# Optimization experiments

Measured on AMD Instinct MI355X. Metric: run time of the kernel, lower is better.

Reference implementation:

```python
import jax, jax.numpy as jnp
import numpy as np

N_NODES = 50000
N_EDGES = 800000
IN_FEATS = 128
H_FEATS = 128
OUT_FEATS = 64


def _mean_agg(h, src, dst, n_nodes):
    # mean over in-neighbors: sum h[src] into dst, divide by in-degree (0 for isolated nodes)
    summed = jax.ops.segment_sum(h[src], dst, num_segments=n_nodes)  # [N, d]
    deg = jax.ops.segment_sum(jnp.ones((src.shape[0],), h.dtype), dst, num_segments=n_nodes)
    return summed / jnp.maximum(deg, 1.0)[:, None]


def setup_inputs() -> dict:
    key = jax.random.key(0)
    ks = jax.random.split(key, 10)
    s = 0.05
    return {
        "inputs": jax.random.normal(ks[0], (N_NODES, IN_FEATS), jnp.float32),
        "fc_W": jax.random.normal(ks[1], (H_FEATS, IN_FEATS), jnp.float32) * s,
        "fc_b": jax.random.normal(ks[2], (H_FEATS,), jnp.float32) * s,
        "W": jax.random.normal(ks[3], (3, H_FEATS, H_FEATS), jnp.float32) * s,
        "b": jax.random.normal(ks[4], (3, H_FEATS), jnp.float32) * s,
        "W_last": jax.random.normal(ks[5], (OUT_FEATS, H_FEATS), jnp.float32) * s,
        "b_last": jax.random.normal(ks[6], (OUT_FEATS,), jnp.float32) * s,
        "eps": jnp.zeros((4,), jnp.float32),
        "src": jax.random.randint(ks[7], (N_EDGES,), 0, N_NODES, jnp.int32),
        "dst": jax.random.randint(ks[8], (N_EDGES,), 0, N_NODES, jnp.int32),
    }


def reference(inputs, fc_W, fc_b, W, b, W_last, b_last, eps, src, dst):
    n = inputs.shape[0]
    # input SLP
    h = jax.nn.relu(inputs @ fc_W.T + fc_b)
    # 3 hidden GIN layers: relu(Linear((1+eps)*h + mean_agg(h)))  (dropout = eval identity)
    for i in range(3):
        agg = _mean_agg(h, src, dst, n)
        h = jax.nn.relu(((1.0 + eps[i]) * h + agg) @ W[i].T + b[i])
    # last GIN layer (no ReLU)
    agg = _mean_agg(h, src, dst, n)
    h = ((1.0 + eps[3]) * h + agg) @ W_last.T + b_last
    return h
```

## Files before the change

### kernel.cpp

```cpp
#include <hip/hip_runtime.h>

#define N_NODES 50000
#define N_EDGES 800000
#define NBUCK 196
#define CAP 4608
#define EPB 4096
#define NSTRIPE ((N_EDGES + EPB - 1) / EPB)

typedef __attribute__((ext_vector_type(8))) short short8;
typedef __attribute__((ext_vector_type(4))) float float4v;

__device__ inline unsigned short f2bf(float f) {
    unsigned u = __float_as_uint(f);
    unsigned r = u + 0x7fff + ((u >> 16) & 1);
    return (unsigned short)(r >> 16);
}
__device__ inline float bf2f(unsigned short h) {
    return __uint_as_float(((unsigned)h) << 16);
}


__global__ void __launch_bounds__(256) wsplit_init(
    const float* __restrict__ fcW, const float* __restrict__ W, const float* __restrict__ Wl,
    unsigned short* __restrict__ hi, unsigned short* __restrict__ lo, int* __restrict__ cursor) {
    if (blockIdx.x == 0 && threadIdx.x < NBUCK) cursor[threadIdx.x] = threadIdx.x * CAP;
    int i = blockIdx.x * 256 + threadIdx.x;
    float v;
    if (i < 16384) v = fcW[i];
    else if (i < 65536) v = W[i - 16384];
    else if (i < 73728) v = Wl[i - 65536];
    else return;
    unsigned short h = f2bf(v);
    hi[i] = h;
    lo[i] = f2bf(v - bf2f(h));
}


__global__ void bucket_scan(const int* __restrict__ cursor, int* __restrict__ boff,
                            int* __restrict__ row_ptr) {
    __shared__ int sm[256];
    int t = threadIdx.x;
    int v = (t < NBUCK) ? (cursor[t] - t * CAP) : 0;
    sm[t] = v;
    __syncthreads();
    for (int o = 1; o < 256; o <<= 1) {
        int x = sm[t];
        int a = (t >= o) ? sm[t - o] : 0;
        __syncthreads();
        sm[t] = x + a;
        __syncthreads();
    }
    if (t < NBUCK) boff[t] = sm[t] - v;
    if (t == NBUCK - 1) {
        boff[NBUCK] = sm[t];
        row_ptr[N_NODES] = sm[t];
    }
}


template <int COLS, bool RELU, bool WRITE_BF, bool BIAS, bool ASPLIT>
__device__ __forceinline__ void gemm_body(int bx, const float* __restrict__ U,
                                          const unsigned short* __restrict__ Uhi,
                                          const unsigned short* __restrict__ Ulo,
                                          const unsigned short* __restrict__ Whi,
                                          const unsigned short* __restrict__ Wlo,
                                          const float* __restrict__ bias, float* __restrict__ out,
                                          unsigned short* __restrict__ outbf, int nrows) {
    int wave = threadIdx.x >> 6;
    int lane = threadIdx.x & 63;
    int m = lane & 15;
    int quad = lane >> 4;
    int r0 = bx * 64 + wave * 16;
    int rowA = r0 + m;
    if (rowA >= nrows) rowA = nrows - 1;

    short8 ahi[4], alo[4];
    if (ASPLIT) {
        const unsigned short* hp = Uhi + (size_t)rowA * 128 + quad * 8;
        const unsigned short* lp = Ulo + (size_t)rowA * 128 + quad * 8;
#pragma unroll
        for (int kc = 0; kc < 4; kc++) {
            ahi[kc] = *(const short8*)(hp + kc * 32);
            alo[kc] = *(const short8*)(lp + kc * 32);
        }
    } else {
        const float* arow = U + (size_t)rowA * 128 + quad * 8;
#pragma unroll
        for (int kc = 0; kc < 4; kc++) {
            float4 f0 = *(const float4*)(arow + kc * 32);
            float4 f1 = *(const float4*)(arow + kc * 32 + 4);
            float fv[8] = {f0.x, f0.y, f0.z, f0.w, f1.x, f1.y, f1.z, f1.w};
#pragma unroll
            for (int j = 0; j < 8; j++) {
                unsigned short h = f2bf(fv[j]);
                ahi[kc][j] = (short)h;
                alo[kc][j] = (short)f2bf(fv[j] - bf2f(h));
            }
        }
    }

#pragma unroll
    for (int nt = 0; nt < COLS / 16; nt++) {
        int n = nt * 16 + m;
        const unsigned short* bhp = Whi + (size_t)n * 128 + quad * 8;
        const unsigned short* blp = Wlo + (size_t)n * 128 + quad * 8;
        float4v acc = {0.f, 0.f, 0.f, 0.f};
#pragma unroll
        for (int kc = 0; kc < 4; kc++) {
            short8 bh = *(const short8*)(bhp + kc * 32);
            short8 bl = *(const short8*)(blp + kc * 32);
            acc = __builtin_amdgcn_mfma_f32_16x16x32_bf16(ahi[kc], bh, acc, 0, 0, 0);
            acc = __builtin_amdgcn_mfma_f32_16x16x32_bf16(alo[kc], bh, acc, 0, 0, 0);
            acc = __builtin_amdgcn_mfma_f32_16x16x32_bf16(ahi[kc], bl, acc, 0, 0, 0);
        }
        float bv = 0.f;
        if (BIAS) bv = bias[n];
#pragma unroll
        for (int i = 0; i < 4; i++) {
            int r = r0 + quad * 4 + i;
            if (r < nrows) {
                float v = acc[i] + bv;
                if (RELU) v = fmaxf(v, 0.f);
                out[(size_t)r * COLS + n] = v;
                if (WRITE_BF) outbf[(size_t)r * COLS + n] = f2bf(v);
            }
        }
    }
}

template <int COLS, bool RELU, bool WRITE_BF, bool BIAS, bool ASPLIT>
__global__ void __launch_bounds__(256) gemm_mfma(const float* __restrict__ U,
                                                 const unsigned short* __restrict__ Uhi,
                                                 const unsigned short* __restrict__ Ulo,
                                                 const unsigned short* __restrict__ Whi,
                                                 const unsigned short* __restrict__ Wlo,
                                                 const float* __restrict__ bias,
                                                 float* __restrict__ out,
                                                 unsigned short* __restrict__ outbf, int nrows) {
    gemm_body<COLS, RELU, WRITE_BF, BIAS, ASPLIT>(blockIdx.x, U, Uhi, Ulo, Whi, Wlo, bias, out,
                                                  outbf, nrows);
}


__global__ void __launch_bounds__(256) fused_binA_gemm(
    const int* __restrict__ src, const int* __restrict__ dst, int* __restrict__ cursor,
    int* __restrict__ packed, const float* __restrict__ X, const unsigned short* __restrict__ whi,
    const unsigned short* __restrict__ wlo, const float* __restrict__ fcb, float* __restrict__ h,
    unsigned short* __restrict__ hbf) {
    int bx = blockIdx.x;
    if (bx < NSTRIPE) {
        __shared__ int lcount[256];
        __shared__ int lbase[256];
        int t = threadIdx.x;
        lcount[t] = 0;
        __syncthreads();
        int base = bx * EPB + t;
#pragma unroll 4
        for (int k = 0; k < EPB / 256; k++) {
            int i = base + k * 256;
            if (i < N_EDGES) atomicAdd(&lcount[((unsigned)dst[i]) >> 8], 1);
        }
        __syncthreads();
        if (t < NBUCK) {
            lbase[t] = atomicAdd(&cursor[t], lcount[t]);
            lcount[t] = 0;
        }
        __syncthreads();
#pragma unroll 4
        for (int k = 0; k < EPB / 256; k++) {
            int i = base + k * 256;
            if (i < N_EDGES) {
                int d = dst[i];
                int wb = ((unsigned)d) >> 8;
                int p = lbase[wb] + atomicAdd(&lcount[wb], 1);
                if (p < (wb + 1) * CAP)
                    packed[p] = ((d & 255) << 16) | src[i];
            }
        }
    } else {
        gemm_body<128, true, true, true, false>(bx - NSTRIPE, X, nullptr, nullptr, whi, wlo, fcb,
                                                h, hbf, N_NODES);
    }
}


__global__ void __launch_bounds__(256) binB_kernel(const int* __restrict__ packed,
                                                   const int* __restrict__ cursor,
                                                   const int* __restrict__ boff,
                                                   int* __restrict__ row_ptr,
                                                   int* __restrict__ esrc) {
    __shared__ int sm[256];
    __shared__ int curs[256];
    int b = blockIdx.x;
    int t = threadIdx.x;
    int e0r = b * CAP, e1r = cursor[b];
    int w0 = boff[b];
    curs[t] = 0;
    __syncthreads();
    for (int i = e0r + t; i < e1r; i += 256) atomicAdd(&curs[((unsigned)packed[i]) >> 16], 1);
    __syncthreads();
    int v = curs[t];
    sm[t] = v;
    __syncthreads();
    for (int o = 1; o < 256; o <<= 1) {
        int x = sm[t];
        int a = (t >= o) ? sm[t - o] : 0;
        __syncthreads();
        sm[t] = x + a;
        __syncthreads();
    }
    int excl = sm[t] - v;
    curs[t] = excl;
    int node = b * 256 + t;
    if (node < N_NODES) row_ptr[node] = w0 + excl;
    __syncthreads();
    for (int i = e0r + t; i < e1r; i += 256) {
        unsigned w = (unsigned)packed[i];
        int p = atomicAdd(&curs[w >> 16], 1);
        esrc[w0 + p] = (int)(w & 0xFFFFu);
    }
}


__global__ void __launch_bounds__(256) agg_kernel(
    const float* __restrict__ h, const unsigned short* __restrict__ hbf,
    const int* __restrict__ row_ptr, const int* __restrict__ esrc,
    const float* __restrict__ eps, int layer, unsigned* __restrict__ uhi32,
    unsigned* __restrict__ ulo32) {
    int gtid = blockIdx.x * 256 + threadIdx.x;
    int node = gtid >> 6;
    int lane = threadIdx.x & 63;
    if (node >= N_NODES) return;
    node = __builtin_amdgcn_readfirstlane(node);
    int beg = __builtin_amdgcn_readfirstlane(row_ptr[node]);
    int end = __builtin_amdgcn_readfirstlane(row_ptr[node + 1]);
    int eg = lane >> 4;
    int fo = lane & 15;

    float acc[8] = {0.f, 0.f, 0.f, 0.f, 0.f, 0.f, 0.f, 0.f};
    int e = beg;
#pragma unroll 2
    for (; e + 3 < end; e += 4) {
        int s = esrc[e + eg];
        short8 v = *(const short8*)(hbf + (size_t)s * 128 + fo * 8);
#pragma unroll
        for (int j = 0; j < 8; j++) acc[j] += bf2f((unsigned short)v[j]);
    }
    int rem = end - e;
    if (eg < rem) {
        int s = esrc[e + eg];
        short8 v = *(const short8*)(hbf + (size_t)s * 128 + fo * 8);
#pragma unroll
        for (int j = 0; j < 8; j++) acc[j] += bf2f((unsigned short)v[j]);
    }
#pragma unroll
    for (int j = 0; j < 8; j++) {
        acc[j] += __shfl_xor(acc[j], 16);
        acc[j] += __shfl_xor(acc[j], 32);
    }
    if (eg == 0) {
        int d = end - beg;
        float inv = (d > 0) ? 1.0f / (float)d : 0.0f;
        float ep = 1.0f + eps[layer];
        const float* hr = h + (size_t)node * 128 + fo * 8;
        float4 h0 = *(const float4*)hr;
        float4 h1 = *(const float4*)(hr + 4);
        float hv[8] = {h0.x, h0.y, h0.z, h0.w, h1.x, h1.y, h1.z, h1.w};
        unsigned hip[4], lop[4];
#pragma unroll
        for (int jj = 0; jj < 4; jj++) {
            float ux = ep * hv[2 * jj] + acc[2 * jj] * inv;
            float uy = ep * hv[2 * jj + 1] + acc[2 * jj + 1] * inv;
            unsigned short uh0 = f2bf(ux), uh1 = f2bf(uy);
            hip[jj] = (unsigned)uh0 | ((unsigned)uh1 << 16);
            lop[jj] = (unsigned)f2bf(ux - bf2f(uh0)) | ((unsigned)f2bf(uy - bf2f(uh1)) << 16);
        }
        uint4* ph = (uint4*)(uhi32 + (size_t)node * 64 + fo * 4);
        uint4* pl = (uint4*)(ulo32 + (size_t)node * 64 + fo * 4);
        *ph = make_uint4(hip[0], hip[1], hip[2], hip[3]);
        *pl = make_uint4(lop[0], lop[1], lop[2], lop[3]);
    }
}


__global__ void __launch_bounds__(256) agg64_out(
    const float* __restrict__ g, const unsigned short* __restrict__ gbf,
    const int* __restrict__ row_ptr, const int* __restrict__ esrc,
    const float* __restrict__ eps, const float* __restrict__ bl, float* __restrict__ out) {
    int gtid = blockIdx.x * 256 + threadIdx.x;
    int node = gtid >> 6;
    if (node >= N_NODES) return;
    int lane = threadIdx.x & 63;
    node = __builtin_amdgcn_readfirstlane(node);
    int beg = __builtin_amdgcn_readfirstlane(row_ptr[node]);
    int end = __builtin_amdgcn_readfirstlane(row_ptr[node + 1]);
    int eg = lane >> 3;
    int fo = lane & 7;

    float acc[8] = {0.f, 0.f, 0.f, 0.f, 0.f, 0.f, 0.f, 0.f};
    int e = beg;
#pragma unroll 2
    for (; e + 7 < end; e += 8) {
        int s = esrc[e + eg];
        short8 v = *(const short8*)(gbf + (size_t)s * 64 + fo * 8);
#pragma unroll
        for (int j = 0; j < 8; j++) acc[j] += bf2f((unsigned short)v[j]);
    }
    int rem = end - e;
    if (eg < rem) {
        int s = esrc[e + eg];
        short8 v = *(const short8*)(gbf + (size_t)s * 64 + fo * 8);
#pragma unroll
        for (int j = 0; j < 8; j++) acc[j] += bf2f((unsigned short)v[j]);
    }
#pragma unroll
    for (int j = 0; j < 8; j++) {
        acc[j] += __shfl_xor(acc[j], 8);
        acc[j] += __shfl_xor(acc[j], 16);
        acc[j] += __shfl_xor(acc[j], 32);
    }
    if (eg == 0) {
        int d = end - beg;
        float inv = (d > 0) ? 1.0f / (float)d : 0.0f;
        float ep = 1.0f + eps[3];
        const float* gr = g + (size_t)node * 64 + fo * 8;
        float4 g0 = *(const float4*)gr;
        float4 g1 = *(const float4*)(gr + 4);
        const float* blr = bl + fo * 8;
        float4 b0 = *(const float4*)blr;
        float4 b1 = *(const float4*)(blr + 4);
        float4 r0, r1;
        r0.x = ep * g0.x + acc[0] * inv + b0.x;
        r0.y = ep * g0.y + acc[1] * inv + b0.y;
        r0.z = ep * g0.z + acc[2] * inv + b0.z;
        r0.w = ep * g0.w + acc[3] * inv + b0.w;
        r1.x = ep * g1.x + acc[4] * inv + b1.x;
        r1.y = ep * g1.y + acc[5] * inv + b1.y;
        r1.z = ep * g1.z + acc[6] * inv + b1.z;
        r1.w = ep * g1.w + acc[7] * inv + b1.w;
        float* op = out + (size_t)node * 64 + fo * 8;
        *(float4*)op = r0;
        *(float4*)(op + 4) = r1;
    }
}


extern "C" void kernel_launch(void* const* d_in, const int* in_sizes, int n_in,
                              void* d_out, int out_size, void* d_ws, size_t ws_size,
                              hipStream_t stream) {
    const float* X   = (const float*)d_in[0];
    const float* fcW = (const float*)d_in[1];
    const float* fcb = (const float*)d_in[2];
    const float* W   = (const float*)d_in[3];
    const float* b   = (const float*)d_in[4];
    const float* Wl  = (const float*)d_in[5];
    const float* bl  = (const float*)d_in[6];
    const float* eps = (const float*)d_in[7];
    const int* src   = (const int*)d_in[8];
    const int* dst   = (const int*)d_in[9];
    float* out = (float*)d_out;

    float* h = (float*)d_ws;
    unsigned short* hbf = (unsigned short*)(h + (size_t)N_NODES * 128);
    unsigned short* uhi = hbf + (size_t)N_NODES * 128;
    unsigned short* ulo = uhi + (size_t)N_NODES * 128;
    unsigned short* whi = ulo + (size_t)N_NODES * 128;
    unsigned short* wlo = whi + 73728;
    int* cursor  = (int*)(wlo + 73728);
    int* boff    = cursor + NBUCK;
    int* row_ptr = boff + NBUCK + 1;
    int* packed  = row_ptr + N_NODES + 1;
    int* esrc    = packed + NBUCK * CAP;
    float* g = (float*)uhi;
    unsigned short* gbf = ulo;

    const int gemm_blocks = (N_NODES + 63) / 64;
    const int agg_blocks = (N_NODES * 64 + 255) / 256;
    const int prep_blocks = (73728 + 255) / 256;

    wsplit_init<<<prep_blocks, 256, 0, stream>>>(fcW, W, Wl, whi, wlo, cursor);
    fused_binA_gemm<<<NSTRIPE + gemm_blocks, 256, 0, stream>>>(src, dst, cursor, packed, X, whi,
                                                               wlo, fcb, h, hbf);
    bucket_scan<<<1, 256, 0, stream>>>(cursor, boff, row_ptr);
    binB_kernel<<<NBUCK, 256, 0, stream>>>(packed, cursor, boff, row_ptr, esrc);

    for (int i = 0; i < 3; i++) {
        agg_kernel<<<agg_blocks, 256, 0, stream>>>(h, hbf, row_ptr, esrc, eps, i,
                                                   (unsigned*)uhi, (unsigned*)ulo);
        if (i < 2)
            gemm_mfma<128, true, true, true, true><<<gemm_blocks, 256, 0, stream>>>(
                nullptr, uhi, ulo, whi + 16384 + (size_t)i * 16384,
                wlo + 16384 + (size_t)i * 16384, b + (size_t)i * 128, h, hbf, N_NODES);
        else
            gemm_mfma<128, true, false, true, true><<<gemm_blocks, 256, 0, stream>>>(
                nullptr, uhi, ulo, whi + 16384 + (size_t)i * 16384,
                wlo + 16384 + (size_t)i * 16384, b + (size_t)i * 128, h, nullptr, N_NODES);
    }

    gemm_mfma<64, false, true, false, false><<<gemm_blocks, 256, 0, stream>>>(
        h, nullptr, nullptr, whi + 65536, wlo + 65536, nullptr, g, gbf, N_NODES);
    agg64_out<<<agg_blocks, 256, 0, stream>>>(g, gbf, row_ptr, esrc, eps, bl, out);
}
```

Before: 403.8 us.

## Fold bucket scan into binB, pad cursors, halve stripe size, dual-accumulate aggregation

Removes the single-block bucket_scan launch by having every binB block redo the 196-entry prefix scan itself. Cursors are now per-bucket counts spaced 16 ints apart and zeroed with a memset, so global atomics no longer share cache lines. Edge stripes shrink to 2048 edges and dst is cached in registers to avoid a second load. The aggregation kernels issue two independent gathers per iteration into separate accumulators to raise memory-level parallelism. The cost is redundant scan work in every binB block, an extra memset, and more register use in the aggregation kernels.

```diff
diff --git a/kernel.cpp b/kernel.cpp
--- a/kernel.cpp
+++ b/kernel.cpp
@@ -4,7 +4,8 @@
 #define N_EDGES 800000
 #define NBUCK 196
 #define CAP 4608
-#define EPB 4096
+#define CSTRIDE 16
+#define EPB 2048
 #define NSTRIPE ((N_EDGES + EPB - 1) / EPB)
 
 typedef __attribute__((ext_vector_type(8))) short short8;
@@ -22,8 +23,7 @@
 
 __global__ void __launch_bounds__(256) wsplit_init(
     const float* __restrict__ fcW, const float* __restrict__ W, const float* __restrict__ Wl,
-    unsigned short* __restrict__ hi, unsigned short* __restrict__ lo, int* __restrict__ cursor) {
-    if (blockIdx.x == 0 && threadIdx.x < NBUCK) cursor[threadIdx.x] = threadIdx.x * CAP;
+    unsigned short* __restrict__ hi, unsigned short* __restrict__ lo) {
     int i = blockIdx.x * 256 + threadIdx.x;
     float v;
     if (i < 16384) v = fcW[i];
@@ -33,28 +33,6 @@
     unsigned short h = f2bf(v);
     hi[i] = h;
     lo[i] = f2bf(v - bf2f(h));
-}
-
-
-__global__ void bucket_scan(const int* __restrict__ cursor, int* __restrict__ boff,
-                            int* __restrict__ row_ptr) {
-    __shared__ int sm[256];
-    int t = threadIdx.x;
-    int v = (t < NBUCK) ? (cursor[t] - t * CAP) : 0;
-    sm[t] = v;
-    __syncthreads();
-    for (int o = 1; o < 256; o <<= 1) {
-        int x = sm[t];
-        int a = (t >= o) ? sm[t - o] : 0;
-        __syncthreads();
-        sm[t] = x + a;
-        __syncthreads();
-    }
-    if (t < NBUCK) boff[t] = sm[t] - v;
-    if (t == NBUCK - 1) {
-        boff[NBUCK] = sm[t];
-        row_ptr[N_NODES] = sm[t];
-    }
 }
 
 
@@ -155,26 +133,27 @@
         lcount[t] = 0;
         __syncthreads();
         int base = bx * EPB + t;
-#pragma unroll 4
+        int d[EPB / 256];
+#pragma unroll
         for (int k = 0; k < EPB / 256; k++) {
             int i = base + k * 256;
-            if (i < N_EDGES) atomicAdd(&lcount[((unsigned)dst[i]) >> 8], 1);
+            d[k] = (i < N_EDGES) ? dst[i] : -1;
+            if (d[k] >= 0) atomicAdd(&lcount[((unsigned)d[k]) >> 8], 1);
         }
         __syncthreads();
         if (t < NBUCK) {
-            lbase[t] = atomicAdd(&cursor[t], lcount[t]);
+            lbase[t] = t * CAP + atomicAdd(&cursor[t * CSTRIDE], lcount[t]);
             lcount[t] = 0;
         }
         __syncthreads();
-#pragma unroll 4
+#pragma unroll
         for (int k = 0; k < EPB / 256; k++) {
-            int i = base + k * 256;
-            if (i < N_EDGES) {
-                int d = dst[i];
-                int wb = ((unsigned)d) >> 8;
+            if (d[k] >= 0) {
+                int i = base + k * 256;
+                int wb = ((unsigned)d[k]) >> 8;
                 int p = lbase[wb] + atomicAdd(&lcount[wb], 1);
                 if (p < (wb + 1) * CAP)
-                    packed[p] = ((d & 255) << 16) | src[i];
+                    packed[p] = ((d[k] & 255) << 16) | src[i];
             }
         }
     } else {
@@ -186,15 +165,30 @@
 
 __global__ void __launch_bounds__(256) binB_kernel(const int* __restrict__ packed,
                                                    const int* __restrict__ cursor,
-                                                   const int* __restrict__ boff,
                                                    int* __restrict__ row_ptr,
                                                    int* __restrict__ esrc) {
     __shared__ int sm[256];
+    __shared__ int cntS[256];
     __shared__ int curs[256];
     int b = blockIdx.x;
     int t = threadIdx.x;
-    int e0r = b * CAP, e1r = cursor[b];
-    int w0 = boff[b];
+    int cnt = (t < NBUCK) ? cursor[t * CSTRIDE] : 0;
+    cntS[t] = cnt;
+    sm[t] = cnt;
+    __syncthreads();
+    for (int o = 1; o < 256; o <<= 1) {
+        int x = sm[t];
+        int a = (t >= o) ? sm[t - o] : 0;
+        __syncthreads();
+        sm[t] = x + a;
+        __syncthreads();
+    }
+    int w0 = sm[b] - cntS[b];
+    int mycnt = cntS[b];
+    int total = sm[NBUCK - 1];
+    __syncthreads();
+    if (b == NBUCK - 1 && t == 0) row_ptr[N_NODES] = total;
+    int e0r = b * CAP, e1r = b * CAP + mycnt;
     curs[t] = 0;
     __syncthreads();
     for (int i = e0r + t; i < e1r; i += 256) atomicAdd(&curs[((unsigned)packed[i]) >> 16], 1);
@@ -238,23 +232,35 @@
     int fo = lane & 15;
 
     float acc[8] = {0.f, 0.f, 0.f, 0.f, 0.f, 0.f, 0.f, 0.f};
+    float acc2[8] = {0.f, 0.f, 0.f, 0.f, 0.f, 0.f, 0.f, 0.f};
     int e = beg;
-#pragma unroll 2
-    for (; e + 3 < end; e += 4) {
+    for (; e + 7 < end; e += 8) {
+        int s0 = esrc[e + eg];
+        int s1 = esrc[e + 4 + eg];
+        short8 v0 = *(const short8*)(hbf + (size_t)s0 * 128 + fo * 8);
+        short8 v1 = *(const short8*)(hbf + (size_t)s1 * 128 + fo * 8);
+#pragma unroll
+        for (int j = 0; j < 8; j++) acc[j] += bf2f((unsigned short)v0[j]);
+#pragma unroll
+        for (int j = 0; j < 8; j++) acc2[j] += bf2f((unsigned short)v1[j]);
+    }
+    if (e + 3 < end) {
         int s = esrc[e + eg];
         short8 v = *(const short8*)(hbf + (size_t)s * 128 + fo * 8);
 #pragma unroll
         for (int j = 0; j < 8; j++) acc[j] += bf2f((unsigned short)v[j]);
+        e += 4;
     }
     int rem = end - e;
     if (eg < rem) {
         int s = esrc[e + eg];
         short8 v = *(const short8*)(hbf + (size_t)s * 128 + fo * 8);
 #pragma unroll
-        for (int j = 0; j < 8; j++) acc[j] += bf2f((unsigned short)v[j]);
+        for (int j = 0; j < 8; j++) acc2[j] += bf2f((unsigned short)v[j]);
     }
 #pragma unroll
     for (int j = 0; j < 8; j++) {
+        acc[j] += acc2[j];
         acc[j] += __shfl_xor(acc[j], 16);
         acc[j] += __shfl_xor(acc[j], 32);
     }
@@ -298,23 +304,35 @@
     int fo = lane & 7;
 
     float acc[8] = {0.f, 0.f, 0.f, 0.f, 0.f, 0.f, 0.f, 0.f};
+    float acc2[8] = {0.f, 0.f, 0.f, 0.f, 0.f, 0.f, 0.f, 0.f};
     int e = beg;
-#pragma unroll 2
-    for (; e + 7 < end; e += 8) {
+    for (; e + 15 < end; e += 16) {
+        int s0 = esrc[e + eg];
+        int s1 = esrc[e + 8 + eg];
+        short8 v0 = *(const short8*)(gbf + (size_t)s0 * 64 + fo * 8);
+        short8 v1 = *(const short8*)(gbf + (size_t)s1 * 64 + fo * 8);
+#pragma unroll
+        for (int j = 0; j < 8; j++) acc[j] += bf2f((unsigned short)v0[j]);
+#pragma unroll
+        for (int j = 0; j < 8; j++) acc2[j] += bf2f((unsigned short)v1[j]);
+    }
+    if (e + 7 < end) {
         int s = esrc[e + eg];
         short8 v = *(const short8*)(gbf + (size_t)s * 64 + fo * 8);
 #pragma unroll
         for (int j = 0; j < 8; j++) acc[j] += bf2f((unsigned short)v[j]);
+        e += 8;
     }
     int rem = end - e;
     if (eg < rem) {
         int s = esrc[e + eg];
         short8 v = *(const short8*)(gbf + (size_t)s * 64 + fo * 8);
 #pragma unroll
-        for (int j = 0; j < 8; j++) acc[j] += bf2f((unsigned short)v[j]);
+        for (int j = 0; j < 8; j++) acc2[j] += bf2f((unsigned short)v[j]);
     }
 #pragma unroll
     for (int j = 0; j < 8; j++) {
+        acc[j] += acc2[j];
         acc[j] += __shfl_xor(acc[j], 8);
         acc[j] += __shfl_xor(acc[j], 16);
         acc[j] += __shfl_xor(acc[j], 32);
@@ -367,8 +385,7 @@
     unsigned short* whi = ulo + (size_t)N_NODES * 128;
     unsigned short* wlo = whi + 73728;
     int* cursor  = (int*)(wlo + 73728);
-    int* boff    = cursor + NBUCK;
-    int* row_ptr = boff + NBUCK + 1;
+    int* row_ptr = cursor + NBUCK * CSTRIDE;
     int* packed  = row_ptr + N_NODES + 1;
     int* esrc    = packed + NBUCK * CAP;
     float* g = (float*)uhi;
@@ -378,11 +395,11 @@
     const int agg_blocks = (N_NODES * 64 + 255) / 256;
     const int prep_blocks = (73728 + 255) / 256;
 
-    wsplit_init<<<prep_blocks, 256, 0, stream>>>(fcW, W, Wl, whi, wlo, cursor);
+    hipMemsetAsync(cursor, 0, NBUCK * CSTRIDE * sizeof(int), stream);
+    wsplit_init<<<prep_blocks, 256, 0, stream>>>(fcW, W, Wl, whi, wlo);
     fused_binA_gemm<<<NSTRIPE + gemm_blocks, 256, 0, stream>>>(src, dst, cursor, packed, X, whi,
                                                                wlo, fcb, h, hbf);
-    bucket_scan<<<1, 256, 0, stream>>>(cursor, boff, row_ptr);
-    binB_kernel<<<NBUCK, 256, 0, stream>>>(packed, cursor, boff, row_ptr, esrc);
+    binB_kernel<<<NBUCK, 256, 0, stream>>>(packed, cursor, row_ptr, esrc);
 
     for (int i = 0; i < 3; i++) {
         agg_kernel<<<agg_blocks, 256, 0, stream>>>(h, hbf, row_ptr, esrc, eps, i,
```

New measurement: 410.3 us. Within noise of the previous version (+1.6%).
